# Kernel optimization log

Measured on AMD Instinct MI355X. Metric: run time of the kernel, lower is better.

The kernel has to match this reference:

```python
import jax, jax.numpy as jnp
import numpy as np


def setup_inputs() -> dict:
    key = jax.random.key(0)
    B, C, L = 8, 32, 131072
    x = jax.random.normal(key, (B, C, L), dtype=jnp.float32)
    return {"x": x, "kernel_size": 9}


def reference(x, kernel_size):
    # x: [B, C, L]; replicate-pad last dim by (k-1)//2 on each side,
    # take sliding windows of size k, return per-window median.
    k = kernel_size
    p = (k - 1) // 2
    L = x.shape[-1]
    xp = jnp.pad(x, ((0, 0), (0, 0), (p, p)), mode="edge")  # [B, C, L+k-1]
    # Stack k shifted views -> [k, B, C, L] (loop over small fixed k only)
    win = jnp.stack([xp[..., i:i + L] for i in range(k)], axis=0)
    # k is odd, so the exact middle of the sorted window is the median
    # (matches torch.median's lower-median convention for odd k).
    return jnp.sort(win, axis=0)[k // 2]
```

## Files before the change

### kernel.cpp

```cpp
#include <hip/hip_runtime.h>


typedef float f32x4 __attribute__((ext_vector_type(4)));

__device__ __forceinline__ float min3f(float a, float b, float c) {
    return fminf(fminf(a, b), c);
}
__device__ __forceinline__ float max3f(float a, float b, float c) {
    return fmaxf(fmaxf(a, b), c);
}
__device__ __forceinline__ float med3f(float a, float b, float c) {
    return __builtin_amdgcn_fmed3f(a, b, c);
}

constexpr int kL     = 131072;
constexpr int kTotal = 8 * 32 * kL;

__global__ __launch_bounds__(256)
void med9_f32_kernel(const float* __restrict__ in, float* __restrict__ out) {
    int base = (blockIdx.x * 256 + threadIdx.x) * 8;
    int col  = base & (kL - 1);
    const float* __restrict__ rin = in + (base - col);

    float v[16];
    if (col >= 4 && col + 12 <= kL) {
        f32x4 a = *reinterpret_cast<const f32x4*>(rin + col - 4);
        f32x4 b = *reinterpret_cast<const f32x4*>(rin + col);
        f32x4 c = *reinterpret_cast<const f32x4*>(rin + col + 4);
        f32x4 d = *reinterpret_cast<const f32x4*>(rin + col + 8);
        v[0]  = a.x; v[1]  = a.y; v[2]  = a.z; v[3]  = a.w;
        v[4]  = b.x; v[5]  = b.y; v[6]  = b.z; v[7]  = b.w;
        v[8]  = c.x; v[9]  = c.y; v[10] = c.z; v[11] = c.w;
        v[12] = d.x; v[13] = d.y; v[14] = d.z; v[15] = d.w;
    } else {
#pragma unroll
        for (int j = 0; j < 16; ++j) {
            int idx = col - 4 + j;
            idx = idx < 0 ? 0 : (idx > kL - 1 ? kL - 1 : idx);
            v[j] = rin[idx];
        }
    }

    float lo[14], mi[14], hi[14];
#pragma unroll
    for (int j = 0; j < 14; ++j) {
        lo[j] = min3f(v[j], v[j + 1], v[j + 2]);
        mi[j] = med3f(v[j], v[j + 1], v[j + 2]);
        hi[j] = max3f(v[j], v[j + 1], v[j + 2]);
    }

    float r[8];
#pragma unroll
    for (int t = 0; t < 8; ++t) {
        float P = max3f(lo[t], lo[t + 3], lo[t + 6]);
        float Q = med3f(mi[t], mi[t + 3], mi[t + 6]);
        float R = min3f(hi[t], hi[t + 3], hi[t + 6]);
        r[t] = med3f(P, Q, R);
    }

    f32x4 r0 = { r[0], r[1], r[2], r[3] };
    f32x4 r1 = { r[4], r[5], r[6], r[7] };
    *reinterpret_cast<f32x4*>(out + base)     = r0;
    *reinterpret_cast<f32x4*>(out + base + 4) = r1;
}

extern "C" void kernel_launch(void* const* d_in, const int* in_sizes, int n_in,
                              void* d_out, int out_size, void* d_ws, size_t ws_size,
                              hipStream_t stream) {
    const float* x = (const float*)d_in[0];
    float* out = (float*)d_out;

    int grid = kTotal / (256 * 8);
    med9_f32_kernel<<<grid, 256, 0, stream>>>(x, out);
}
```

Measured before the change: 44.71 us.

## Process four strided 4-wide chunks per thread for coalesced loads and stores

Each thread now handles four chunks of 4 outputs that are spaced 1024 floats apart, instead of 8 contiguous outputs. Neighbouring lanes therefore touch adjacent 16-byte segments, so each load and store instruction is fully coalesced and more loads are in flight per thread. The cost is more halo reads per output (12 inputs for 4 outputs instead of 16 for 8) and more registers per thread.

```diff
diff --git a/kernel.cpp b/kernel.cpp
--- a/kernel.cpp
+++ b/kernel.cpp
@@ -13,55 +13,65 @@
     return __builtin_amdgcn_fmed3f(a, b, c);
 }
 
-constexpr int kL     = 131072;
-constexpr int kTotal = 8 * 32 * kL;
+constexpr int kL      = 131072;
+constexpr int kTotal  = 8 * 32 * kL;
+constexpr int kChunks = 4;
+constexpr int kChunkStride = 256 * 4;
+constexpr int kBlockFloats = kChunks * kChunkStride;
 
 __global__ __launch_bounds__(256)
 void med9_f32_kernel(const float* __restrict__ in, float* __restrict__ out) {
-    int base = (blockIdx.x * 256 + threadIdx.x) * 8;
-    int col  = base & (kL - 1);
-    const float* __restrict__ rin = in + (base - col);
+    int tid   = threadIdx.x;
+    int base0 = blockIdx.x * kBlockFloats + tid * 4;
+    int col0  = base0 & (kL - 1);
+    const float* __restrict__ rin = in + (base0 - col0);
 
-    float v[16];
-    if (col >= 4 && col + 12 <= kL) {
-        f32x4 a = *reinterpret_cast<const f32x4*>(rin + col - 4);
-        f32x4 b = *reinterpret_cast<const f32x4*>(rin + col);
-        f32x4 c = *reinterpret_cast<const f32x4*>(rin + col + 4);
-        f32x4 d = *reinterpret_cast<const f32x4*>(rin + col + 8);
-        v[0]  = a.x; v[1]  = a.y; v[2]  = a.z; v[3]  = a.w;
-        v[4]  = b.x; v[5]  = b.y; v[6]  = b.z; v[7]  = b.w;
-        v[8]  = c.x; v[9]  = c.y; v[10] = c.z; v[11] = c.w;
-        v[12] = d.x; v[13] = d.y; v[14] = d.z; v[15] = d.w;
+    float v[kChunks][12];
+    bool interior = (col0 >= 4) & (col0 + 3 * kChunkStride + 8 <= kL);
+
+    if (interior) {
+#pragma unroll
+        for (int c = 0; c < kChunks; ++c) {
+            int col = col0 + c * kChunkStride;
+            f32x4 a = *reinterpret_cast<const f32x4*>(rin + col - 4);
+            f32x4 b = *reinterpret_cast<const f32x4*>(rin + col);
+            f32x4 d = *reinterpret_cast<const f32x4*>(rin + col + 4);
+            v[c][0] = a.x; v[c][1] = a.y; v[c][2]  = a.z; v[c][3]  = a.w;
+            v[c][4] = b.x; v[c][5] = b.y; v[c][6]  = b.z; v[c][7]  = b.w;
+            v[c][8] = d.x; v[c][9] = d.y; v[c][10] = d.z; v[c][11] = d.w;
+        }
     } else {
 #pragma unroll
-        for (int j = 0; j < 16; ++j) {
-            int idx = col - 4 + j;
-            idx = idx < 0 ? 0 : (idx > kL - 1 ? kL - 1 : idx);
-            v[j] = rin[idx];
+        for (int c = 0; c < kChunks; ++c) {
+            int col = col0 + c * kChunkStride;
+#pragma unroll
+            for (int j = 0; j < 12; ++j) {
+                int idx = col - 4 + j;
+                idx = idx < 0 ? 0 : (idx > kL - 1 ? kL - 1 : idx);
+                v[c][j] = rin[idx];
+            }
         }
     }
 
-    float lo[14], mi[14], hi[14];
 #pragma unroll
-    for (int j = 0; j < 14; ++j) {
-        lo[j] = min3f(v[j], v[j + 1], v[j + 2]);
-        mi[j] = med3f(v[j], v[j + 1], v[j + 2]);
-        hi[j] = max3f(v[j], v[j + 1], v[j + 2]);
+    for (int c = 0; c < kChunks; ++c) {
+        float lo[10], mi[10], hi[10];
+#pragma unroll
+        for (int j = 0; j < 10; ++j) {
+            lo[j] = min3f(v[c][j], v[c][j + 1], v[c][j + 2]);
+            mi[j] = med3f(v[c][j], v[c][j + 1], v[c][j + 2]);
+            hi[j] = max3f(v[c][j], v[c][j + 1], v[c][j + 2]);
+        }
+        f32x4 r;
+#pragma unroll
+        for (int t = 0; t < 4; ++t) {
+            float P = max3f(lo[t], lo[t + 3], lo[t + 6]);
+            float Q = med3f(mi[t], mi[t + 3], mi[t + 6]);
+            float R = min3f(hi[t], hi[t + 3], hi[t + 6]);
+            ((float*)&r)[t] = med3f(P, Q, R);
+        }
+        *reinterpret_cast<f32x4*>(out + base0 + c * kChunkStride) = r;
     }
-
-    float r[8];
-#pragma unroll
-    for (int t = 0; t < 8; ++t) {
-        float P = max3f(lo[t], lo[t + 3], lo[t + 6]);
-        float Q = med3f(mi[t], mi[t + 3], mi[t + 6]);
-        float R = min3f(hi[t], hi[t + 3], hi[t + 6]);
-        r[t] = med3f(P, Q, R);
-    }
-
-    f32x4 r0 = { r[0], r[1], r[2], r[3] };
-    f32x4 r1 = { r[4], r[5], r[6], r[7] };
-    *reinterpret_cast<f32x4*>(out + base)     = r0;
-    *reinterpret_cast<f32x4*>(out + base + 4) = r1;
 }
 
 extern "C" void kernel_launch(void* const* d_in, const int* in_sizes, int n_in,
@@ -70,6 +80,6 @@
     const float* x = (const float*)d_in[0];
     float* out = (float*)d_out;
 
-    int grid = kTotal / (256 * 8);
+    int grid = kTotal / kBlockFloats;
     med9_f32_kernel<<<grid, 256, 0, stream>>>(x, out);
 }
```

Result: slower. 46.24 us (+3.4%).
